# Optimization experiments

Hardware: AMD Instinct MI355X
Metric: run time of the kernel (lower is better)

The kernel has to match this reference:

```python
import jax, jax.numpy as jnp
import numpy as np

A_MAX = 7  # 2**A_bits - 1 with A_bits=3
W_HI = 7   # torch.randint(0, 2**W_bits - 1) -> values in [0, 6]


def _conv_valid(x, w):
    # x: [N,C,H,W] float32, w: [O,I,kh,kw] float32; stride 1, no padding
    return jax.lax.conv_general_dilated(
        x, w, window_strides=(1, 1), padding='VALID',
        dimension_numbers=('NCHW', 'OIHW', 'NCHW'))


def setup_inputs() -> dict:
    key = jax.random.key(0)
    k_x, k_w = jax.random.split(key)
    x = jax.random.randint(k_x, (16, 64, 112, 112), 0, 8, dtype=jnp.int32)
    # 3-bit weights of the original 7x7 conv, values 0..6
    W7 = jax.random.randint(k_w, (128, 64, 7, 7), 0, W_HI).astype(jnp.float32)
    w1 = W7[:, :, :, 0:3]
    w2 = W7[:, :, :, 2:5]
    w2 = w2.at[:, :, :, 0].set(0.0)
    w2 = w2.at[:, :, :, 2].set(0.0)
    w3 = W7[:, :, :, 4:7]
    return {"x": x, "w1": w1, "w2": w2, "w3": w3}


def reference(x, w1, w2, w3):
    # 3-bit activation quantization: clip int input to [0, 7]
    xc = jnp.clip(x, 0, A_MAX).astype(jnp.float32)
    out1 = _conv_valid(xc[:, :, :, :-2], w1)   # [N,O,H-6,W-4]
    out2 = _conv_valid(xc, w2)                 # [N,O,H-6,W-2]
    out3 = _conv_valid(xc[:, :, :, 2:], w3)    # [N,O,H-6,W-4]
    # combine slices -> equivalent to valid 7x7 conv: [N,O,H-6,W-6]
    return out1[:, :, :, :-2] + out2[:, :, :, 2:-2] + out3[:, :, :, 2:]
```

## Files before the change

### kernel.cpp

```cpp
#include <hip/hip_runtime.h>
#include <cstdint>

typedef __attribute__((ext_vector_type(4))) int i32x4;

#define XROWS  22
#define ROWB   2048
#define WSLICE 8192
#define WB_BYTES 409600
#define XT_BYTES ((size_t)16 * 112 * 128 * 64)
#define NTILES 1568
#define GRID_MAIN 1536

__device__ __forceinline__ void g2lds16(const void* g, void* l) {
  __builtin_amdgcn_global_load_lds(
      (const __attribute__((address_space(1))) unsigned int*)g,
      (__attribute__((address_space(3))) unsigned int*)l, 16, 0, 0);
}

__global__ void prep_w(const float* __restrict__ w1,
                       const float* __restrict__ w2,
                       const float* __restrict__ w3,
                       signed char* __restrict__ wb) {
  int t = blockIdx.x * 256 + threadIdx.x;
  int lo = t & 15;
  int co = (t >> 4) & 127;
  int g  = (t >> 11) & 3;
  int s  = t >> 13;
  if (s >= 49) return;
  int kh = s / 7, kw = s % 7;
  int ci = g * 16 + lo;
  int base = ((co * 64 + ci) * 7 + kh) * 3;
  float v;
  if (kw < 3)       v = w1[base + kw];
  else if (kw == 3) v = w2[base + 1];
  else              v = w3[base + kw - 4];
  wb[t] = (signed char)(int)v;
}

__global__ void prep_xw(const int* __restrict__ x,
                        const float* __restrict__ w1,
                        const float* __restrict__ w2,
                        const float* __restrict__ w3,
                        signed char* __restrict__ xt,
                        signed char* __restrict__ wb) {
  __shared__ unsigned char T[64 * 68];
  const int tid = threadIdx.x;
  const int wt = blockIdx.x * 64, h = blockIdx.y, n = blockIdx.z;
  const int fid = (blockIdx.z * 112 + blockIdx.y) * 2 + blockIdx.x;

  if (fid < 1568) {
    int t = fid * 256 + tid;
    int lo = t & 15;
    int co = (t >> 4) & 127;
    int g  = (t >> 11) & 3;
    int s  = t >> 13;
    int kh = s / 7, kw = s % 7;
    int ci = g * 16 + lo;
    int base = ((co * 64 + ci) * 7 + kh) * 3;
    float v;
    if (kw < 3)       v = w1[base + kw];
    else if (kw == 3) v = w2[base + 1];
    else              v = w3[base + kw - 4];
    wb[t] = (signed char)(int)v;
  }

  {
    const int wr = tid & 63;
    const int cb = (tid >> 6) * 16;
    int ws = wt + wr; ws = ws < 112 ? ws : 111;
    const int* xp = x + (((size_t)n * 64 + cb) * 112 + h) * 112 + ws;
    #pragma unroll
    for (int g4 = 0; g4 < 4; ++g4) {
      uint32_t v = 0;
      #pragma unroll
      for (int j = 0; j < 4; ++j) {
        int a = xp[(g4 * 4 + j) * 12544];
        a = a < 0 ? 0 : (a > 7 ? 7 : a);
        v |= (uint32_t)a << (8 * j);
      }
      *(uint32_t*)&T[wr * 68 + cb + g4 * 4] = v;
    }
  }
  __syncthreads();
  {
    const int wo = tid >> 2, q = tid & 3;
    const int key = ((wt + wo) >> 1) & 3;
    const int sg = (q ^ key) << 4;
    int4 v;
    v.x = *(const int*)&T[wo * 68 + sg + 0];
    v.y = *(const int*)&T[wo * 68 + sg + 4];
    v.z = *(const int*)&T[wo * 68 + sg + 8];
    v.w = *(const int*)&T[wo * 68 + sg + 12];
    *(int4*)&xt[(((size_t)n * 112 + h) * 128 + wt + wo) * 64 + q * 16] = v;
  }
}

#define MFMA(acc, a, b) acc = __builtin_amdgcn_mfma_i32_16x16x64_i8(a, b, acc, 0, 0, 0)

__global__ __launch_bounds__(256, 3)
void conv7s(const signed char* __restrict__ xt,
            const signed char* __restrict__ wb,
            float* __restrict__ out) {
  __shared__ __align__(16) unsigned char Xs[XROWS * ROWB];

  const int tid  = threadIdx.x;
  const int lane = tid & 63;
  const int wid  = tid >> 6;
  const int lrow = lane & 15;
  const int lkg  = lane >> 4;
  const int cop  = wid >> 1;
  const int sph  = wid & 1;
  const int rowB = sph * 8;

  const int L  = blockIdx.x;
  const int Lp = (L & 7) * 192 + (L >> 3);
  const int npass = (L < 32) ? 2 : 1;

  for (int pass = 0; pass < npass; ++pass) {
    const int t = (pass == 0) ? Lp : (GRID_MAIN + L);
    const int coh = t & 1;
    const int r2  = t >> 1;
    const int bx  = r2 % 7;
    const int t7  = r2 / 7;
    const int by  = t7 % 7;
    const int n   = t7 / 7;
    const int ho_base = by * 16;
    const int wo_base = bx * 16;

    const signed char* aB = wb + lkg * 2048 + (coh * 64 + cop * 32 + lrow) * 16;
    i32x4 A[2];
    #pragma unroll
    for (int m = 0; m < 2; ++m) A[m] = *(const i32x4*)(aB + m * 256);

    if (pass) __syncthreads();

    for (int r = wid; r < XROWS; r += 4) {
      int h = ho_base + r; h = h < 112 ? h : 111;
      const signed char* src = xt + (((size_t)n * 112 + h) * 128 + wo_base) * 64;
      g2lds16(src + lane * 16, &Xs[r * ROWB]);
      g2lds16(src + 1024 + lane * 16, &Xs[r * ROWB + 1024]);
    }
    asm volatile("s_waitcnt vmcnt(0)" ::: "memory");
    __syncthreads();

    i32x4 acc[2][8];
    #pragma unroll
    for (int m = 0; m < 2; ++m)
      #pragma unroll
      for (int b = 0; b < 8; ++b)
        acc[m][b] = (i32x4){0, 0, 0, 0};

    for (int kw = 0; kw < 7; ++kw) {
      const int w_l  = lrow + kw;
      const int bcol = w_l * 64 + ((lkg ^ ((w_l >> 1) & 3)) << 4);
      i32x4 B[8];
      #pragma unroll
      for (int b = 0; b < 8; ++b)
        B[b] = *(const i32x4*)&Xs[(rowB + b) * ROWB + bcol];

      #pragma unroll
      for (int kh = 0; kh < 7; ++kh) {
        const signed char* apn = aB + (size_t)(kh < 6 ? (kh + 1) * 7 + kw : kw + 1) * WSLICE;
        __builtin_amdgcn_s_setprio(1);
        #pragma unroll
        for (int m = 0; m < 2; ++m) {
          #pragma unroll
          for (int b = 0; b < 8; ++b)
            MFMA(acc[m][b], A[m], B[(kh + b) & 7]);
          A[m] = *(const i32x4*)(apn + m * 256);
        }
        __builtin_amdgcn_s_setprio(0);
        if (kh < 6)
          B[kh & 7] = *(const i32x4*)&Xs[(rowB + kh + 8) * ROWB + bcol];
      }
    }

    const int wo = wo_base + lrow;
    if (wo < 106) {
      #pragma unroll
      for (int m = 0; m < 2; ++m) {
        const int co = coh * 64 + cop * 32 + m * 16 + lkg * 4;
        #pragma unroll
        for (int b = 0; b < 8; ++b) {
          const int ho = ho_base + rowB + b;
          if (ho < 106) {
            float* op = out + (((size_t)n * 128 + co) * 106 + ho) * 106 + wo;
            #pragma unroll
            for (int j = 0; j < 4; ++j)
              op[(size_t)j * 11236] = (float)acc[m][b][j];
          }
        }
      }
    }
  }
}

__global__ __launch_bounds__(256, 3)
void conv7f(const int* __restrict__ x,
            const signed char* __restrict__ wb, float* __restrict__ out) {
  __shared__ __align__(16) unsigned char Xs[XROWS * ROWB];

  const int tid  = threadIdx.x;
  const int lane = tid & 63;
  const int wid  = tid >> 6;
  const int lrow = lane & 15;
  const int lkg  = lane >> 4;

  const int L  = blockIdx.x;
  const int Lp = (L & 7) * 196 + (L >> 3);
  const int coh = Lp & 1;
  const int r2  = Lp >> 1;
  const int bx  = r2 % 7;
  const int t7  = r2 / 7;
  const int by  = t7 % 7;
  const int n   = t7 / 7;
  const int ho_base = by * 16;
  const int wo_base = bx * 16;

  const signed char* aB = wb + lkg * 2048 + coh * 1024 + lrow * 16;
  i32x4 A[4];
  #pragma unroll
  for (int m = 0; m < 4; ++m) A[m] = *(const i32x4*)(aB + m * 256);

  {
    const int w_a  = tid & 15,       cg_a  = tid >> 4;
    const int w_b2 = 16 + (tid & 7), cg_b2 = tid >> 3;
    const bool doB = (tid < 128) && ((tid & 7) < 6);
    const int keyA = ((w_a >> 1) & 3) << 2;
    const int keyB = ((w_b2 >> 1) & 3) << 2;
    for (int r = 0; r < XROWS; ++r) {
      int h = ho_base + r; h = h < 112 ? h : 111;
      const int* xr = x + (size_t)n * 64 * 12544 + h * 112;
      {
        int wc = wo_base + w_a; wc = wc < 112 ? wc : 111;
        uint32_t v = 0;
        #pragma unroll
        for (int j = 0; j < 4; ++j) {
          int a = xr[(cg_a * 4 + j) * 12544 + wc];
          a = a < 0 ? 0 : (a > 7 ? 7 : a);
          v |= (uint32_t)a << (8 * j);
        }
        *(uint32_t*)&Xs[r * ROWB + w_a * 64 + ((cg_a ^ keyA) << 2)] = v;
      }
      if (doB) {
        int wc = wo_base + w_b2; wc = wc < 112 ? wc : 111;
        uint32_t v = 0;
        #pragma unroll
        for (int j = 0; j < 4; ++j) {
          int a = xr[(cg_b2 * 4 + j) * 12544 + wc];
          a = a < 0 ? 0 : (a > 7 ? 7 : a);
          v |= (uint32_t)a << (8 * j);
        }
        *(uint32_t*)&Xs[r * ROWB + w_b2 * 64 + ((cg_b2 ^ keyB) << 2)] = v;
      }
    }
  }
  __syncthreads();

  i32x4 acc[4][4];
  #pragma unroll
  for (int m = 0; m < 4; ++m)
    #pragma unroll
    for (int b = 0; b < 4; ++b)
      acc[m][b] = (i32x4){0, 0, 0, 0};

  const int rowB = wid * 4;

  for (int kw = 0; kw < 7; ++kw) {
    const int w_l  = lrow + kw;
    const int bcol = w_l * 64 + ((lkg ^ ((w_l >> 1) & 3)) << 4);
    i32x4 B[8];
    #pragma unroll
    for (int b = 0; b < 4; ++b)
      B[b] = *(const i32x4*)&Xs[(rowB + b) * ROWB + bcol];
    #pragma unroll
    for (int kh = 0; kh < 7; ++kh) {
      if (kh < 6)
        B[(kh + 4) & 7] = *(const i32x4*)&Xs[(rowB + kh + 4) * ROWB + bcol];
      const signed char* apn = aB + (size_t)(kh < 6 ? (kh + 1) * 7 + kw : kw + 1) * WSLICE;
      #pragma unroll
      for (int m = 0; m < 4; ++m) {
        #pragma unroll
        for (int b = 0; b < 4; ++b)
          MFMA(acc[m][b], A[m], B[(kh + b) & 7]);
        A[m] = *(const i32x4*)(apn + m * 256);
      }
    }
  }

  const int wo = wo_base + lrow;
  if (wo < 106) {
    #pragma unroll
    for (int m = 0; m < 4; ++m) {
      const int co = coh * 64 + m * 16 + lkg * 4;
      #pragma unroll
      for (int b = 0; b < 4; ++b) {
        const int ho = ho_base + rowB + b;
        if (ho < 106) {
          float* op = out + (((size_t)n * 128 + co) * 106 + ho) * 106 + wo;
          #pragma unroll
          for (int j = 0; j < 4; ++j)
            op[(size_t)j * 11236] = (float)acc[m][b][j];
        }
      }
    }
  }
}

extern "C" void kernel_launch(void* const* d_in, const int* in_sizes, int n_in,
                              void* d_out, int out_size, void* d_ws, size_t ws_size,
                              hipStream_t stream) {
  const int*   x  = (const int*)d_in[0];
  const float* w1 = (const float*)d_in[1];
  const float* w2 = (const float*)d_in[2];
  const float* w3 = (const float*)d_in[3];
  float* outp = (float*)d_out;
  signed char* wbp = (signed char*)d_ws;
  signed char* xtp = wbp + WB_BYTES;

  if (ws_size >= WB_BYTES + XT_BYTES) {
    prep_xw<<<dim3(2, 112, 16), dim3(256), 0, stream>>>(x, w1, w2, w3, xtp, wbp);
    conv7s<<<dim3(GRID_MAIN), dim3(256), 0, stream>>>(xtp, wbp, outp);
  } else {
    prep_w<<<dim3(1568), dim3(256), 0, stream>>>(w1, w2, w3, wbp);
    conv7f<<<dim3(1568), dim3(256), 0, stream>>>(x, wbp, outp);
  }
}
```

Measured before the change: 75.03 us.

## Reassign each wave to one 16-channel tile across all 16 output rows

Each wave now covers a single 16-output-channel slice for all 16 output rows, instead of two 16-channel slices for 8 rows. This halves the per-wave weight fragment loads from global memory and uses a two-register ping-pong to prefetch them. In exchange, each wave reads more input rows from LDS per kw step (16+6 instead of 8+6), and each B fragment feeds one MFMA chain instead of two. The last-kw prefetch index is clamped so it never reads past the weight buffer.

New measurement: 70.95 us. 5.4% less time.

```diff
diff --git a/kernel.cpp b/kernel.cpp
--- a/kernel.cpp
+++ b/kernel.cpp
@@ -108,9 +108,6 @@
   const int wid  = tid >> 6;
   const int lrow = lane & 15;
   const int lkg  = lane >> 4;
-  const int cop  = wid >> 1;
-  const int sph  = wid & 1;
-  const int rowB = sph * 8;
 
   const int L  = blockIdx.x;
   const int Lp = (L & 7) * 192 + (L >> 3);
@@ -127,10 +124,10 @@
     const int ho_base = by * 16;
     const int wo_base = bx * 16;
 
-    const signed char* aB = wb + lkg * 2048 + (coh * 64 + cop * 32 + lrow) * 16;
-    i32x4 A[2];
-    #pragma unroll
-    for (int m = 0; m < 2; ++m) A[m] = *(const i32x4*)(aB + m * 256);
+    const signed char* aB = wb + lkg * 2048 + (coh * 64 + wid * 16 + lrow) * 16;
+
+    i32x4 Aa = *(const i32x4*)aB;
+    i32x4 Ab;
 
     if (pass) __syncthreads();
 
@@ -143,52 +140,52 @@
     asm volatile("s_waitcnt vmcnt(0)" ::: "memory");
     __syncthreads();
 
-    i32x4 acc[2][8];
-    #pragma unroll
-    for (int m = 0; m < 2; ++m)
-      #pragma unroll
-      for (int b = 0; b < 8; ++b)
-        acc[m][b] = (i32x4){0, 0, 0, 0};
+    i32x4 acc[16];
+    #pragma unroll
+    for (int j = 0; j < 16; ++j) acc[j] = (i32x4){0, 0, 0, 0};
 
     for (int kw = 0; kw < 7; ++kw) {
       const int w_l  = lrow + kw;
       const int bcol = w_l * 64 + ((lkg ^ ((w_l >> 1) & 3)) << 4);
-      i32x4 B[8];
-      #pragma unroll
-      for (int b = 0; b < 8; ++b)
-        B[b] = *(const i32x4*)&Xs[(rowB + b) * ROWB + bcol];
+      i32x4 B[16];
+      #pragma unroll
+      for (int b = 0; b < 16; ++b)
+        B[b] = *(const i32x4*)&Xs[b * ROWB + bcol];
 
       #pragma unroll
       for (int kh = 0; kh < 7; ++kh) {
-        const signed char* apn = aB + (size_t)(kh < 6 ? (kh + 1) * 7 + kw : kw + 1) * WSLICE;
+        const signed char* apn =
+            aB + (size_t)(kh < 6 ? (kh + 1) * 7 + kw : (kw < 6 ? kw + 1 : 0)) * WSLICE;
         __builtin_amdgcn_s_setprio(1);
-        #pragma unroll
-        for (int m = 0; m < 2; ++m) {
+        if ((kh & 1) == 0) {
+          Ab = *(const i32x4*)apn;
           #pragma unroll
-          for (int b = 0; b < 8; ++b)
-            MFMA(acc[m][b], A[m], B[(kh + b) & 7]);
-          A[m] = *(const i32x4*)(apn + m * 256);
+          for (int j = 0; j < 16; ++j)
+            MFMA(acc[j], Aa, B[(kh + j) & 15]);
+        } else {
+          Aa = *(const i32x4*)apn;
+          #pragma unroll
+          for (int j = 0; j < 16; ++j)
+            MFMA(acc[j], Ab, B[(kh + j) & 15]);
         }
         __builtin_amdgcn_s_setprio(0);
         if (kh < 6)
-          B[kh & 7] = *(const i32x4*)&Xs[(rowB + kh + 8) * ROWB + bcol];
-      }
+          B[kh] = *(const i32x4*)&Xs[(kh + 16) * ROWB + bcol];
+      }
+      Aa = Ab;
     }
 
     const int wo = wo_base + lrow;
     if (wo < 106) {
-      #pragma unroll
-      for (int m = 0; m < 2; ++m) {
-        const int co = coh * 64 + cop * 32 + m * 16 + lkg * 4;
-        #pragma unroll
-        for (int b = 0; b < 8; ++b) {
-          const int ho = ho_base + rowB + b;
-          if (ho < 106) {
-            float* op = out + (((size_t)n * 128 + co) * 106 + ho) * 106 + wo;
-            #pragma unroll
-            for (int j = 0; j < 4; ++j)
-              op[(size_t)j * 11236] = (float)acc[m][b][j];
-          }
+      const int co = coh * 64 + wid * 16 + lkg * 4;
+      #pragma unroll
+      for (int j = 0; j < 16; ++j) {
+        const int ho = ho_base + j;
+        if (ho < 106) {
+          float* op = out + (((size_t)n * 128 + co) * 106 + ho) * 106 + wo;
+          #pragma unroll
+          for (int jj = 0; jj < 4; ++jj)
+            op[(size_t)jj * 11236] = (float)acc[j][jj];
         }
       }
     }
```
